# Performance work log

Hardware: AMD Instinct MI355X
Metric: run time of the kernel (lower is better)

## Reference

```python
import jax, jax.numpy as jnp
import numpy as np

B, S, D, H, DK, F, K = 8, 1024, 512, 8, 64, 2048, 31
EPS = 1e-5


def _ln(x, g, b):
    m = jnp.mean(x, -1, keepdims=True)
    v = jnp.mean((x - m) ** 2, -1, keepdims=True)
    return (x - m) * jax.lax.rsqrt(v + EPS) * g + b


def _ff(x, w1, b1, w2, b2):
    return jnp.maximum(x @ w1 + b1, 0.0) @ w2 + b2


def setup_inputs() -> dict:
    key = jax.random.key(0)
    ks = jax.random.split(key, 16)
    w = lambda k, shape: jax.random.normal(k, shape, dtype=jnp.float32) * 0.02
    inp = {"x": jax.random.normal(ks[0], (B, S, D), dtype=jnp.float32)}
    for name in ["norm1", "norm2", "norm3", "norm4", "conv_ln"]:
        inp[name + "_g"] = jnp.ones((D,), jnp.float32)
        inp[name + "_b"] = jnp.zeros((D,), jnp.float32)
    # feed-forward 1 and 2
    inp["ff1_w1"] = w(ks[1], (D, F)); inp["ff1_b1"] = jnp.zeros((F,), jnp.float32)
    inp["ff1_w2"] = w(ks[2], (F, D)); inp["ff1_b2"] = jnp.zeros((D,), jnp.float32)
    inp["ff2_w1"] = w(ks[3], (D, F)); inp["ff2_b1"] = jnp.zeros((F,), jnp.float32)
    inp["ff2_w2"] = w(ks[4], (F, D)); inp["ff2_b2"] = jnp.zeros((D,), jnp.float32)
    # attention projections ([in, out] layout)
    inp["wq"] = w(ks[5], (D, D)); inp["bq"] = jnp.zeros((D,), jnp.float32)
    inp["wk"] = w(ks[6], (D, D)); inp["bk"] = jnp.zeros((D,), jnp.float32)
    inp["wv"] = w(ks[7], (D, D)); inp["bv"] = jnp.zeros((D,), jnp.float32)
    inp["wo"] = w(ks[8], (D, D)); inp["bo"] = jnp.zeros((D,), jnp.float32)
    # convolution module
    inp["pw1_w"] = w(ks[9], (D, 2 * D)); inp["pw1_b"] = jnp.zeros((2 * D,), jnp.float32)
    inp["dw_w"] = w(ks[10], (D, 1, K)); inp["dw_b"] = jnp.zeros((D,), jnp.float32)
    inp["bn_g"] = jnp.ones((D,), jnp.float32); inp["bn_b"] = jnp.zeros((D,), jnp.float32)
    inp["bn_mean"] = jnp.zeros((D,), jnp.float32); inp["bn_var"] = jnp.ones((D,), jnp.float32)
    inp["pw2_w"] = w(ks[11], (D, D)); inp["pw2_b"] = jnp.zeros((D,), jnp.float32)
    return inp


def _forward(x, norm1_g, norm1_b, norm2_g, norm2_b, norm3_g, norm3_b, norm4_g, norm4_b,
             ff1_w1, ff1_b1, ff1_w2, ff1_b2, wq, bq, wk, bk, wv, bv, wo, bo,
             conv_ln_g, conv_ln_b, pw1_w, pw1_b, dw_w, dw_b,
             bn_g, bn_b, bn_mean, bn_var, pw2_w, pw2_b,
             ff2_w1, ff2_b1, ff2_w2, ff2_b2):
    b, s, _ = x.shape
    # half-step FF1
    x = x + 0.5 * _ff(_ln(x, norm1_g, norm1_b), ff1_w1, ff1_b1, ff1_w2, ff1_b2)
    # multi-head self-attention (pre-norm)
    h = _ln(x, norm2_g, norm2_b)
    q = (h @ wq + bq).reshape(b, s, H, DK)
    k = (h @ wk + bk).reshape(b, s, H, DK)
    v = (h @ wv + bv).reshape(b, s, H, DK)
    scores = jnp.einsum("bqhd,bkhd->bhqk", q, k) / jnp.sqrt(jnp.asarray(DK, x.dtype))
    attn = jax.nn.softmax(scores, axis=-1)
    o = jnp.einsum("bhqk,bkhd->bqhd", attn, v).reshape(b, s, D)
    x = x + (o @ wo + bo)
    # convolution module (pre-norm)
    h = _ln(x, norm3_g, norm3_b)
    h = _ln(h, conv_ln_g, conv_ln_b)
    h = h @ pw1_w + pw1_b                                 # [B,S,2D] pointwise conv1
    h = h[..., :D] * jax.nn.sigmoid(h[..., D:])           # GLU over channels
    h = h.transpose(0, 2, 1)                              # [B,D,S]
    h = jax.lax.conv_general_dilated(
        h, dw_w, window_strides=(1,), padding=((K // 2, K // 2),),
        feature_group_count=D, dimension_numbers=("NCH", "OIH", "NCH")) + dw_b[:, None]
    h = (h - bn_mean[:, None]) * jax.lax.rsqrt(bn_var + EPS)[:, None] * bn_g[:, None] + bn_b[:, None]
    h = h * jax.nn.sigmoid(h)                             # SiLU
    h = jnp.einsum("bcl,co->bol", h, pw2_w) + pw2_b[:, None]
    x = x + h.transpose(0, 2, 1)
    # half-step FF2
    x = x + 0.5 * _ff(_ln(x, norm4_g, norm4_b), ff2_w1, ff2_b1, ff2_w2, ff2_b2)
    return x


def reference(x, norm1_g, norm1_b, norm2_g, norm2_b, norm3_g, norm3_b, norm4_g, norm4_b,
              conv_ln_g, conv_ln_b, ff1_w1, ff1_b1, ff1_w2, ff1_b2,
              ff2_w1, ff2_b1, ff2_w2, ff2_b2, wq, bq, wk, bk, wv, bv, wo, bo,
              pw1_w, pw1_b, dw_w, dw_b, bn_g, bn_b, bn_mean, bn_var, pw2_w, pw2_b):
    return _forward(x, norm1_g, norm1_b, norm2_g, norm2_b, norm3_g, norm3_b, norm4_g, norm4_b,
                    ff1_w1, ff1_b1, ff1_w2, ff1_b2, wq, bq, wk, bk, wv, bv, wo, bo,
                    conv_ln_g, conv_ln_b, pw1_w, pw1_b, dw_w, dw_b,
                    bn_g, bn_b, bn_mean, bn_var, pw2_w, pw2_b,
                    ff2_w1, ff2_b1, ff2_w2, ff2_b2)
```

## Files before the change

### kernel.cpp

```cpp
#include <hip/hip_runtime.h>
#include <math.h>

#define TOK    8192
#define DMODEL 512
#define FDIM   2048
#define NH     8
#define DKH    64
#define SEQ    1024
#define BATCH  8
#define KCONV  31
#define LN_EPS 1e-5f

typedef __attribute__((ext_vector_type(8))) short bf16x8;
typedef __attribute__((ext_vector_type(4))) float f32x4;
typedef unsigned short ushort_t;

#define AS1 __attribute__((address_space(1)))
#define AS3 __attribute__((address_space(3)))

#define QSCALE 0.1803368801111204f

__device__ __forceinline__ float sigf(float x) { return 1.0f / (1.0f + __expf(-x)); }

__device__ __forceinline__ unsigned short f2bf(float f) {
  unsigned u = __float_as_uint(f);
  u = u + 0x7fffu + ((u >> 16) & 1u);
  return (unsigned short)(u >> 16);
}
__device__ __forceinline__ unsigned pk2(float a, float b) {
  return (unsigned)f2bf(a) | ((unsigned)f2bf(b) << 16);
}
__device__ __forceinline__ float bf2f(ushort_t u) {
  return __uint_as_float((unsigned)u << 16);
}

__device__ __forceinline__ void xcd_swizzle(int gx, int* bx, int* by) {
  const int nwg = gx * (int)gridDim.y;
  const int cpx = nwg >> 3;
  const int bid = (*by) * gx + (*bx);
  const int wg = (bid & 7) * cpx + (bid >> 3);
  *bx = wg % gx;
  *by = wg / gx;
}

struct WJob { const float* src; ushort_t* dst; int K, N, t0; };
struct WJobs {
  WJob j[10];
  int misc_t0;
  const float* dww; const float* bq; const float* bk; const float* bv;
  float* wTc; float* bcat;
};

__global__ __launch_bounds__(256) void wcast_all(WJobs jobs) {
  __shared__ float tile[32][33];
  const int t = blockIdx.x;
  const int tx = threadIdx.x, ty = threadIdx.y;
  if (t >= jobs.misc_t0) {
    const int idx = (t - jobs.misc_t0) * 256 + ty * 32 + tx;
    if (idx < DMODEL * KCONV) {
      const int d = idx / KCONV, k = idx % KCONV;
      jobs.wTc[k * DMODEL + d] = jobs.dww[idx];
    } else if (idx < DMODEL * KCONV + 3 * DMODEL) {
      const int c = idx - DMODEL * KCONV;
      jobs.bcat[c] = (c < DMODEL) ? jobs.bq[c]
                    : (c < 2 * DMODEL ? jobs.bk[c - DMODEL] : jobs.bv[c - 2 * DMODEL]);
    }
    return;
  }
  int i = 0;
#pragma unroll
  for (int k = 1; k < 10; ++k) if (t >= jobs.j[k].t0) i = k;
  const WJob jb = jobs.j[i];
  const int local = t - jb.t0;
  const int ntx = jb.N >> 5;
  const int bx = (local % ntx) * 32, by = (local / ntx) * 32;
#pragma unroll
  for (int r = 0; r < 32; r += 8)
    tile[ty + r][tx] = jb.src[(size_t)(by + ty + r) * jb.N + bx + tx];
  __syncthreads();
#pragma unroll
  for (int r = 0; r < 32; r += 8)
    jb.dst[(size_t)(bx + ty + r) * jb.K + by + tx] = f2bf(tile[tx][ty + r]);
}

template <bool OBF>
__global__ __launch_bounds__(256) void ln_kernel(const float* __restrict__ in,
                                                 const float* __restrict__ g,
                                                 const float* __restrict__ b,
                                                 void* __restrict__ outp) {
  const int wave = threadIdx.x >> 6, lane = threadIdx.x & 63;
  const size_t row = (size_t)blockIdx.x * 4 + wave;
  const float* p = in + row * DMODEL + lane * 8;
  const float4 v0 = *(const float4*)p;
  const float4 v1 = *(const float4*)(p + 4);
  float s  = v0.x + v0.y + v0.z + v0.w + v1.x + v1.y + v1.z + v1.w;
  float ss = v0.x*v0.x + v0.y*v0.y + v0.z*v0.z + v0.w*v0.w
           + v1.x*v1.x + v1.y*v1.y + v1.z*v1.z + v1.w*v1.w;
#pragma unroll
  for (int m = 1; m < 64; m <<= 1) { s += __shfl_xor(s, m); ss += __shfl_xor(ss, m); }
  const float mean = s * (1.0f / DMODEL);
  const float var  = ss * (1.0f / DMODEL) - mean * mean;
  const float rstd = rsqrtf(var + LN_EPS);
  const float4 g0 = *(const float4*)(g + lane * 8);
  const float4 g1 = *(const float4*)(g + lane * 8 + 4);
  const float4 bb0 = *(const float4*)(b + lane * 8);
  const float4 bb1 = *(const float4*)(b + lane * 8 + 4);
  float o[8];
  o[0] = (v0.x - mean) * rstd * g0.x + bb0.x;
  o[1] = (v0.y - mean) * rstd * g0.y + bb0.y;
  o[2] = (v0.z - mean) * rstd * g0.z + bb0.z;
  o[3] = (v0.w - mean) * rstd * g0.w + bb0.w;
  o[4] = (v1.x - mean) * rstd * g1.x + bb1.x;
  o[5] = (v1.y - mean) * rstd * g1.y + bb1.y;
  o[6] = (v1.z - mean) * rstd * g1.z + bb1.z;
  o[7] = (v1.w - mean) * rstd * g1.w + bb1.w;
  if (OBF) {
    uint4 pkv;
    pkv.x = pk2(o[0], o[1]); pkv.y = pk2(o[2], o[3]);
    pkv.z = pk2(o[4], o[5]); pkv.w = pk2(o[6], o[7]);
    *(uint4*)((ushort_t*)outp + row * DMODEL + lane * 8) = pkv;
  } else {
    float4 a, c;
    a.x = o[0]; a.y = o[1]; a.z = o[2]; a.w = o[3];
    c.x = o[4]; c.y = o[5]; c.z = o[6]; c.w = o[7];
    float* q = (float*)outp + row * DMODEL + lane * 8;
    *(float4*)q = a;
    *(float4*)(q + 4) = c;
  }
}

__global__ __launch_bounds__(256) void ln2_kernel(const float* __restrict__ in,
                                                  const float* __restrict__ g1,
                                                  const float* __restrict__ b1,
                                                  const float* __restrict__ g2,
                                                  const float* __restrict__ b2,
                                                  ushort_t* __restrict__ outp) {
  const int wave = threadIdx.x >> 6, lane = threadIdx.x & 63;
  const size_t row = (size_t)blockIdx.x * 4 + wave;
  const float* p = in + row * DMODEL + lane * 8;
  float v[8];
  {
    const float4 v0 = *(const float4*)p;
    const float4 v1 = *(const float4*)(p + 4);
    v[0]=v0.x; v[1]=v0.y; v[2]=v0.z; v[3]=v0.w;
    v[4]=v1.x; v[5]=v1.y; v[6]=v1.z; v[7]=v1.w;
  }
  float s = 0.f, ss = 0.f;
#pragma unroll
  for (int e = 0; e < 8; ++e) { s += v[e]; ss += v[e]*v[e]; }
#pragma unroll
  for (int m = 1; m < 64; m <<= 1) { s += __shfl_xor(s, m); ss += __shfl_xor(ss, m); }
  float mean = s * (1.0f / DMODEL);
  float rstd = rsqrtf(ss * (1.0f / DMODEL) - mean * mean + LN_EPS);
  const float4 ga = *(const float4*)(g1 + lane * 8);
  const float4 gb = *(const float4*)(g1 + lane * 8 + 4);
  const float4 ba = *(const float4*)(b1 + lane * 8);
  const float4 bb = *(const float4*)(b1 + lane * 8 + 4);
  const float gg1[8] = {ga.x,ga.y,ga.z,ga.w,gb.x,gb.y,gb.z,gb.w};
  const float bb1[8] = {ba.x,ba.y,ba.z,ba.w,bb.x,bb.y,bb.z,bb.w};
#pragma unroll
  for (int e = 0; e < 8; ++e) v[e] = (v[e] - mean) * rstd * gg1[e] + bb1[e];
  s = 0.f; ss = 0.f;
#pragma unroll
  for (int e = 0; e < 8; ++e) { s += v[e]; ss += v[e]*v[e]; }
#pragma unroll
  for (int m = 1; m < 64; m <<= 1) { s += __shfl_xor(s, m); ss += __shfl_xor(ss, m); }
  mean = s * (1.0f / DMODEL);
  rstd = rsqrtf(ss * (1.0f / DMODEL) - mean * mean + LN_EPS);
  const float4 gc = *(const float4*)(g2 + lane * 8);
  const float4 gd = *(const float4*)(g2 + lane * 8 + 4);
  const float4 bc = *(const float4*)(b2 + lane * 8);
  const float4 bd = *(const float4*)(b2 + lane * 8 + 4);
  const float gg2[8] = {gc.x,gc.y,gc.z,gc.w,gd.x,gd.y,gd.z,gd.w};
  const float bb2[8] = {bc.x,bc.y,bc.z,bc.w,bd.x,bd.y,bd.z,bd.w};
  float o[8];
#pragma unroll
  for (int e = 0; e < 8; ++e) o[e] = (v[e] - mean) * rstd * gg2[e] + bb2[e];
  uint4 pkv;
  pkv.x = pk2(o[0], o[1]); pkv.y = pk2(o[2], o[3]);
  pkv.z = pk2(o[4], o[5]); pkv.w = pk2(o[6], o[7]);
  *(uint4*)(outp + row * DMODEL + lane * 8) = pkv;
}

template <int ACT, bool QSC>
__global__ __launch_bounds__(512, 2) void gemm256(const ushort_t* __restrict__ A,
                                                  const ushort_t* __restrict__ Bt,
                                                  const float* __restrict__ bias,
                                                  ushort_t* __restrict__ Cout,
                                                  int N) {
  __shared__ ushort_t lds[65536];
  const int t = threadIdx.x;
  const int l = t & 63;
  const int wid = t >> 6;
  const int wm = wid >> 2, wn = wid & 3;
  int bx = blockIdx.x, by = blockIdx.y;
  xcd_swizzle(gridDim.x, &bx, &by);
  const int m0 = by * 256, n0 = bx * 256;
  const int K = 512;

  f32x4 acc[8][4];
#pragma unroll
  for (int m = 0; m < 8; ++m)
#pragma unroll
    for (int n = 0; n < 4; ++n) acc[m][n] = (f32x4){0.f, 0.f, 0.f, 0.f};

  const int srow = t >> 3;
  const int schunk = (t & 7) ^ ((t >> 3) & 7);

#define STAGE_A(TAU, C_, I_)                                                    \
  __builtin_amdgcn_global_load_lds(                                             \
      (const AS1 unsigned*)(A + (size_t)(m0 + (I_) * 64 + srow) * K +           \
                            (TAU) * 64 + schunk * 8),                           \
      (AS3 unsigned*)(lds + (C_) * 16384 + ((I_) * 512 + t) * 8), 16, 0, 0)
#define STAGE_B(TAU, C_, I_)                                                    \
  __builtin_amdgcn_global_load_lds(                                             \
      (const AS1 unsigned*)(Bt + (size_t)(n0 + (I_) * 64 + srow) * K +          \
                            (TAU) * 64 + schunk * 8),                           \
      (AS3 unsigned*)(lds + 32768 + (C_) * 16384 + ((I_) * 512 + t) * 8), 16, 0, 0)

#pragma unroll
  for (int i = 0; i < 4; ++i) STAGE_B(0, 0, i);
#pragma unroll
  for (int i = 0; i < 4; ++i) STAGE_A(0, 0, i);
#pragma unroll
  for (int i = 0; i < 4; ++i) STAGE_B(1, 1, i);
  STAGE_A(1, 1, 0);
  STAGE_A(1, 1, 2);
  asm volatile("s_waitcnt vmcnt(6)" ::: "memory");
  __builtin_amdgcn_s_barrier();

  const int arow = (l & 15);
  const int kch0 = (l >> 4);
  bf16x8 bfr[2][4];

  for (int it = 0; it < 4; ++it) {
    const bool stg = (it < 3);
#pragma unroll
    for (int h = 0; h < 2; ++h) {
      const int c = h;
#pragma unroll
      for (int p = 0; p < 4; ++p) {
        bf16x8 afr[2][2];
#pragma unroll
        for (int m2 = 0; m2 < 2; ++m2)
#pragma unroll
          for (int ks = 0; ks < 2; ++ks) {
            const int row = wm * 128 + (2 * p + m2) * 16 + arow;
            const int ch = (ks * 4 + kch0) ^ (row & 7);
            afr[m2][ks] = *(const bf16x8*)(lds + c * 16384 + row * 64 + ch * 8);
          }
        if (p == 0) {
#pragma unroll
          for (int nr = 0; nr < 4; ++nr)
#pragma unroll
            for (int ks = 0; ks < 2; ++ks) {
              const int row = wn * 64 + nr * 16 + arow;
              const int ch = (ks * 4 + kch0) ^ (row & 7);
              bfr[ks][nr] = *(const bf16x8*)(lds + 32768 + c * 16384 + row * 64 + ch * 8);
            }
        }
        if (p == 0) {
          if (h == 0 || stg) {
            STAGE_A(2 * it + h + 1, c ^ 1, 1);
            STAGE_A(2 * it + h + 1, c ^ 1, 3);
          }
        } else if (p == 1) {
          if (stg) {
#pragma unroll
            for (int i = 0; i < 4; ++i) STAGE_B(2 * it + h + 2, c, i);
          }
        } else if (p == 2) {
          if (stg) {
            STAGE_A(2 * it + h + 2, c, 0);
            STAGE_A(2 * it + h + 2, c, 2);
          }
        }
        __builtin_amdgcn_s_barrier();
        __builtin_amdgcn_s_setprio(1);
#pragma unroll
        for (int ks = 0; ks < 2; ++ks)
#pragma unroll
          for (int m2 = 0; m2 < 2; ++m2)
#pragma unroll
            for (int nr = 0; nr < 4; ++nr)
              acc[2 * p + m2][nr] = __builtin_amdgcn_mfma_f32_16x16x32_bf16(
                  afr[m2][ks], bfr[ks][nr], acc[2 * p + m2][nr], 0, 0, 0);
        __builtin_amdgcn_s_setprio(0);
        if (p == 3) {
          if (h == 0) {
            if (stg) asm volatile("s_waitcnt vmcnt(6)" ::: "memory");
            else     asm volatile("s_waitcnt vmcnt(0)" ::: "memory");
          } else if (stg) {
            asm volatile("s_waitcnt vmcnt(6)" ::: "memory");
          }
        }
        __builtin_amdgcn_s_barrier();
      }
    }
  }
#undef STAGE_A
#undef STAGE_B

#pragma unroll
  for (int m = 0; m < 8; ++m) {
    const int row_b = m0 + wm * 128 + m * 16 + (l >> 4) * 4;
#pragma unroll
    for (int n = 0; n < 4; ++n) {
      const int col = n0 + wn * 64 + n * 16 + (l & 15);
      const float bv = bias[col];
      const float sc = QSC ? (col < DMODEL ? QSCALE : 1.0f) : 1.0f;
#pragma unroll
      for (int j = 0; j < 4; ++j) {
        float v = acc[m][n][j] + bv;
        if (ACT == 1) v = fmaxf(v, 0.f);
        v *= sc;
        Cout[(size_t)(row_b + j) * N + col] = f2bf(v);
      }
    }
  }
}

template <int TN, int ACT, bool RES, bool OBF, bool QSC>
__global__ __launch_bounds__(256) void gemm_bf16(const ushort_t* __restrict__ A,
                                                 const ushort_t* __restrict__ Bt,
                                                 const float* __restrict__ bias,
                                                 const float* __restrict__ Rp,
                                                 float alpha,
                                                 void* __restrict__ Cout,
                                                 int M, int N, int K) {
  constexpr int NF = TN / 32;
  constexpr int NB = TN / 32;
  __shared__ ushort_t Al[128 * 64];
  __shared__ ushort_t Bl[TN * 64];
  const int t = threadIdx.x;
  const int lane = t & 63;
  const int wid = t >> 6;
  const int wr = wid >> 1, wc = wid & 1;
  int bx = blockIdx.x, by = blockIdx.y;
  xcd_swizzle(gridDim.x, &bx, &by);
  const int m0 = by * 128, n0 = bx * TN;

  f32x4 acc[4][NF];
#pragma unroll
  for (int m = 0; m < 4; ++m)
#pragma unroll
    for (int n = 0; n < NF; ++n) acc[m][n] = (f32x4){0.f, 0.f, 0.f, 0.f};

  const int srow = t >> 3;
  const int scol = (t & 7) * 8;
  const ushort_t* Ag = A + (size_t)(m0 + srow) * K + scol;
  const ushort_t* Bg = Bt + (size_t)(n0 + srow) * K + scol;

  for (int k0 = 0; k0 < K; k0 += 64) {
    __syncthreads();
#pragma unroll
    for (int i = 0; i < 4; ++i) {
      __builtin_amdgcn_global_load_lds(
          (const AS1 unsigned*)(Ag + (size_t)i * 32 * K + k0),
          (AS3 unsigned*)(Al + ((size_t)i * 256 + t) * 8),
          16, 0, 0);
    }
#pragma unroll
    for (int i = 0; i < NB; ++i) {
      __builtin_amdgcn_global_load_lds(
          (const AS1 unsigned*)(Bg + (size_t)i * 32 * K + k0),
          (AS3 unsigned*)(Bl + ((size_t)i * 256 + t) * 8),
          16, 0, 0);
    }
    __syncthreads();

#pragma unroll
    for (int ks = 0; ks < 2; ++ks) {
      const int kk = ks * 32 + (lane >> 4) * 8;
      bf16x8 af[4], bfv[NF];
#pragma unroll
      for (int m = 0; m < 4; ++m)
        af[m] = *(const bf16x8*)(Al + (wr * 64 + m * 16 + (lane & 15)) * 64 + kk);
#pragma unroll
      for (int n = 0; n < NF; ++n)
        bfv[n] = *(const bf16x8*)(Bl + (wc * (TN / 2) + n * 16 + (lane & 15)) * 64 + kk);
#pragma unroll
      for (int m = 0; m < 4; ++m)
#pragma unroll
        for (int n = 0; n < NF; ++n)
          acc[m][n] = __builtin_amdgcn_mfma_f32_16x16x32_bf16(af[m], bfv[n], acc[m][n], 0, 0, 0);
    }
  }

#pragma unroll
  for (int m = 0; m < 4; ++m) {
    const int row_b = m0 + wr * 64 + m * 16 + (lane >> 4) * 4;
#pragma unroll
    for (int n = 0; n < NF; ++n) {
      const int col = n0 + wc * (TN / 2) + n * 16 + (lane & 15);
      const float bv = bias[col];
#pragma unroll
      for (int j = 0; j < 4; ++j) {
        float v = acc[m][n][j] + bv;
        if (ACT == 1) v = fmaxf(v, 0.f);
        if (QSC) v *= (col < DMODEL ? QSCALE : 1.0f);
        const size_t idx = (size_t)(row_b + j) * N + col;
        if (RES) v = Rp[idx] + alpha * v;
        if (OBF) ((ushort_t*)Cout)[idx] = f2bf(v);
        else     ((float*)Cout)[idx] = v;
      }
    }
  }
}

__global__ __launch_bounds__(256) void gemm_glu(const ushort_t* __restrict__ A,
                                                const ushort_t* __restrict__ Bt,
                                                const float* __restrict__ bias,
                                                ushort_t* __restrict__ Cout) {
  __shared__ ushort_t Al[128 * 64];
  __shared__ ushort_t Bl[128 * 64];
  const int t = threadIdx.x;
  const int lane = t & 63;
  const int wid = t >> 6;
  const int wr = wid >> 1, wc = wid & 1;
  int bx = blockIdx.x, by = blockIdx.y;
  xcd_swizzle(gridDim.x, &bx, &by);
  const int m0 = by * 128, n0 = bx * 64;
  const int K = DMODEL, N = DMODEL;

  f32x4 aa[4][2], ag[4][2];
#pragma unroll
  for (int m = 0; m < 4; ++m)
#pragma unroll
    for (int n = 0; n < 2; ++n) {
      aa[m][n] = (f32x4){0.f, 0.f, 0.f, 0.f};
      ag[m][n] = (f32x4){0.f, 0.f, 0.f, 0.f};
    }

  const int srow = t >> 3;
  const int scol = (t & 7) * 8;
  const ushort_t* Ag_ = A + (size_t)(m0 + srow) * K + scol;
  const ushort_t* Ba_ = Bt + (size_t)(n0 + srow) * K + scol;
  const ushort_t* Bg_ = Bt + (size_t)(512 + n0 + srow) * K + scol;

  for (int k0 = 0; k0 < K; k0 += 64) {
    __syncthreads();
#pragma unroll
    for (int i = 0; i < 4; ++i) {
      __builtin_amdgcn_global_load_lds(
          (const AS1 unsigned*)(Ag_ + (size_t)i * 32 * K + k0),
          (AS3 unsigned*)(Al + ((size_t)i * 256 + t) * 8),
          16, 0, 0);
    }
#pragma unroll
    for (int i = 0; i < 2; ++i) {
      __builtin_amdgcn_global_load_lds(
          (const AS1 unsigned*)(Ba_ + (size_t)i * 32 * K + k0),
          (AS3 unsigned*)(Bl + ((size_t)i * 256 + t) * 8),
          16, 0, 0);
      __builtin_amdgcn_global_load_lds(
          (const AS1 unsigned*)(Bg_ + (size_t)i * 32 * K + k0),
          (AS3 unsigned*)(Bl + 64 * 64 + ((size_t)i * 256 + t) * 8),
          16, 0, 0);
    }
    __syncthreads();

#pragma unroll
    for (int ks = 0; ks < 2; ++ks) {
      const int kk = ks * 32 + (lane >> 4) * 8;
      bf16x8 af[4], bfa[2], bfg[2];
#pragma unroll
      for (int m = 0; m < 4; ++m)
        af[m] = *(const bf16x8*)(Al + (wr * 64 + m * 16 + (lane & 15)) * 64 + kk);
#pragma unroll
      for (int n = 0; n < 2; ++n) {
        bfa[n] = *(const bf16x8*)(Bl + (wc * 32 + n * 16 + (lane & 15)) * 64 + kk);
        bfg[n] = *(const bf16x8*)(Bl + (64 + wc * 32 + n * 16 + (lane & 15)) * 64 + kk);
      }
#pragma unroll
      for (int m = 0; m < 4; ++m)
#pragma unroll
        for (int n = 0; n < 2; ++n) {
          aa[m][n] = __builtin_amdgcn_mfma_f32_16x16x32_bf16(af[m], bfa[n], aa[m][n], 0, 0, 0);
          ag[m][n] = __builtin_amdgcn_mfma_f32_16x16x32_bf16(af[m], bfg[n], ag[m][n], 0, 0, 0);
        }
    }
  }

#pragma unroll
  for (int m = 0; m < 4; ++m) {
    const int row_b = m0 + wr * 64 + m * 16 + (lane >> 4) * 4;
#pragma unroll
    for (int n = 0; n < 2; ++n) {
      const int col = n0 + wc * 32 + n * 16 + (lane & 15);
      const float ba_v = bias[col];
      const float bg_v = bias[col + DMODEL];
#pragma unroll
      for (int j = 0; j < 4; ++j) {
        const float av = aa[m][n][j] + ba_v;
        const float gv = ag[m][n][j] + bg_v;
        Cout[(size_t)(row_b + j) * N + col] = f2bf(av * sigf(gv));
      }
    }
  }
}

__global__ __launch_bounds__(256) void vtrans(const ushort_t* __restrict__ QKV,
                                              ushort_t* __restrict__ Vt) {
  __shared__ ushort_t tl[64][72];
  const int st = blockIdx.x;
  const int bh = blockIdx.y;
  const int b = bh >> 3, h = bh & 7;
  const int t = threadIdx.x;
#pragma unroll
  for (int i = 0; i < 2; ++i) {
    const int chunk = i * 256 + t;
    const int sr = chunk >> 3, c8 = (chunk & 7) * 8;
    *(uint4*)&tl[sr][c8] =
        *(const uint4*)(QKV + ((size_t)(b * SEQ + st * 64 + sr) * (3 * DMODEL)) + 2 * DMODEL + h * DKH + c8);
  }
  __syncthreads();
#pragma unroll
  for (int i = 0; i < 2; ++i) {
    const int chunk = i * 256 + t;
    const int dr = chunk >> 3, c8 = (chunk & 7) * 8;
    ushort_t tmp[8];
#pragma unroll
    for (int e = 0; e < 8; ++e) tmp[e] = tl[c8 + e][dr];
    *(uint4*)(Vt + ((size_t)(bh * DKH + dr) * SEQ) + st * 64 + c8) = *(uint4*)tmp;
  }
}

__global__ __launch_bounds__(256) void attn_mfma(const ushort_t* __restrict__ QKV,
                                                 const ushort_t* __restrict__ Vt,
                                                 ushort_t* __restrict__ Om) {
  __shared__ ushort_t Ks[128 * 64];
  __shared__ ushort_t Vs[64 * 128];
  __shared__ ushort_t Ps[64 * 128];
  const int t = threadIdx.x;
  const int l = t & 63;
  const int w = t >> 6;
  const int qb = blockIdx.x, h = blockIdx.y, b = blockIdx.z;
  const size_t rowstr = 3 * DMODEL;
  const size_t baseQ = ((size_t)b * SEQ) * rowstr + (size_t)h * DKH;
  const size_t baseK = baseQ + DMODEL;
  const size_t baseV = (size_t)(b * NH + h) * DKH * SEQ;
  const size_t baseO = ((size_t)b * SEQ) * DMODEL + (size_t)h * DKH;

  bf16x8 qf[2];
  {
    const int qrow = qb * 64 + w * 16 + (l & 15);
    const ushort_t* qp = QKV + baseQ + (size_t)qrow * rowstr + ((l >> 4) * 8);
    qf[0] = *(const bf16x8*)(qp);
    qf[1] = *(const bf16x8*)(qp + 32);
  }

  const int krr = t >> 3, kch = t & 7;
  const int vrr = t >> 4, vch = t & 15;

  float mrun[4], lrun[4];
  f32x4 o[4];
#pragma unroll
  for (int j = 0; j < 4; ++j) { mrun[j] = -1e30f; lrun[j] = 0.f; }
#pragma unroll
  for (int n = 0; n < 4; ++n) o[n] = (f32x4){0.f, 0.f, 0.f, 0.f};

  for (int kt = 0; kt < SEQ / 128; ++kt) {
    __syncthreads();
#pragma unroll
    for (int i = 0; i < 4; ++i) {
      const int r = i * 32 + krr;
      __builtin_amdgcn_global_load_lds(
          (const AS1 unsigned*)
              (QKV + baseK + (size_t)(kt * 128 + r) * rowstr + ((kch ^ (r & 7)) * 8)),
          (AS3 unsigned*)(Ks + ((size_t)i * 256 + t) * 8),
          16, 0, 0);
    }
#pragma unroll
    for (int i = 0; i < 4; ++i) {
      const int r = i * 16 + vrr;
      __builtin_amdgcn_global_load_lds(
          (const AS1 unsigned*)
              (Vt + baseV + (size_t)r * SEQ + kt * 128 + ((vch ^ (r & 15)) * 8)),
          (AS3 unsigned*)(Vs + ((size_t)i * 256 + t) * 8),
          16, 0, 0);
    }
    __syncthreads();

    f32x4 s[8];
#pragma unroll
    for (int n = 0; n < 8; ++n) s[n] = (f32x4){0.f, 0.f, 0.f, 0.f};
    __builtin_amdgcn_s_setprio(1);
#pragma unroll
    for (int ks = 0; ks < 2; ++ks) {
      const int kk = ks * 64 + (l >> 4) * 16;
#pragma unroll
      for (int n = 0; n < 8; ++n) {
        const int krow = n * 16 + (l & 15);
        const bf16x8 kf = *(const bf16x8*)((char*)Ks + krow * 128 + (kk ^ ((krow & 7) << 4)));
        s[n] = __builtin_amdgcn_mfma_f32_16x16x32_bf16(qf[ks], kf, s[n], 0, 0, 0);
      }
    }
    __builtin_amdgcn_s_setprio(0);

#pragma unroll
    for (int j = 0; j < 4; ++j) {
      float r0 = fmaxf(fmaxf(fmaxf(s[0][j], s[1][j]), fmaxf(s[2][j], s[3][j])),
                       fmaxf(fmaxf(s[4][j], s[5][j]), fmaxf(s[6][j], s[7][j])));
      r0 = fmaxf(r0, __shfl_xor(r0, 1));
      r0 = fmaxf(r0, __shfl_xor(r0, 2));
      r0 = fmaxf(r0, __shfl_xor(r0, 4));
      r0 = fmaxf(r0, __shfl_xor(r0, 8));
      const float mn = fmaxf(mrun[j], r0);
      const float cs = exp2f(mrun[j] - mn);
      const int prow = w * 16 + (l >> 4) * 4 + j;
      const int pswz = (prow & 15) << 4;
      float psum = 0.f;
#pragma unroll
      for (int n = 0; n < 8; ++n) {
        const float p = exp2f(s[n][j] - mn);
        psum += p;
        const int col2 = (n * 16 + (l & 15)) * 2;
        *(ushort_t*)((char*)Ps + prow * 256 + (col2 ^ pswz)) = f2bf(p);
      }
      psum += __shfl_xor(psum, 1);
      psum += __shfl_xor(psum, 2);
      psum += __shfl_xor(psum, 4);
      psum += __shfl_xor(psum, 8);
      lrun[j] = lrun[j] * cs + psum;
      mrun[j] = mn;
      o[0][j] *= cs; o[1][j] *= cs; o[2][j] *= cs; o[3][j] *= cs;
    }

    __builtin_amdgcn_s_setprio(1);
#pragma unroll
    for (int ks = 0; ks < 4; ++ks) {
      const int kk = ks * 64 + (l >> 4) * 16;
      const int arow = w * 16 + (l & 15);
      const bf16x8 pf = *(const bf16x8*)((char*)Ps + arow * 256 + (kk ^ ((arow & 15) << 4)));
#pragma unroll
      for (int n = 0; n < 4; ++n) {
        const int vrow = n * 16 + (l & 15);
        const bf16x8 vf = *(const bf16x8*)((char*)Vs + vrow * 256 + (kk ^ ((vrow & 15) << 4)));
        o[n] = __builtin_amdgcn_mfma_f32_16x16x32_bf16(pf, vf, o[n], 0, 0, 0);
      }
    }
    __builtin_amdgcn_s_setprio(0);
  }

  float inv[4];
#pragma unroll
  for (int j = 0; j < 4; ++j) inv[j] = 1.0f / lrun[j];
#pragma unroll
  for (int j = 0; j < 4; ++j) {
    const int prow = w * 16 + (l >> 4) * 4 + j;
    const int pswz = (prow & 15) << 4;
#pragma unroll
    for (int n = 0; n < 4; ++n) {
      const int col2 = (n * 16 + (l & 15)) * 2;
      *(ushort_t*)((char*)Ps + prow * 256 + (col2 ^ pswz)) = f2bf(o[n][j] * inv[j]);
    }
  }
  __syncthreads();
#pragma unroll
  for (int i = 0; i < 2; ++i) {
    const int chunk = i * 256 + t;
    const int qr = chunk >> 3, c8 = (chunk & 7) * 8;
    const uint4 ov = *(const uint4*)((char*)Ps + qr * 256 + ((c8 * 2) ^ ((qr & 15) << 4)));
    *(uint4*)(Om + baseO + (size_t)(qb * 64 + qr) * DMODEL + c8) = ov;
  }
}

__global__ __launch_bounds__(256) void dwconv_bn_silu(const ushort_t* __restrict__ in,
                                                      const float* __restrict__ wT,
                                                      const float* __restrict__ dwb,
                                                      const float* __restrict__ bng,
                                                      const float* __restrict__ bnb,
                                                      const float* __restrict__ bnm,
                                                      const float* __restrict__ bnv,
                                                      ushort_t* __restrict__ out) {
  const size_t gid = (size_t)blockIdx.x * 256 + threadIdx.x;
  const int dc = (int)(gid & 63) * 8;
  const int s = (int)((gid >> 6) & (SEQ - 1));
  const int b = (int)(gid >> 16);
  const ushort_t* bp = in + (size_t)b * SEQ * DMODEL;
  float a[8];
#pragma unroll
  for (int e = 0; e < 8; ++e) a[e] = 0.f;
#pragma unroll
  for (int k = 0; k < KCONV; ++k) {
    const int ssi = s + k - (KCONV / 2);
    if (ssi < 0 || ssi >= SEQ) continue;
    ushort_t xv[8];
    *(uint4*)xv = *(const uint4*)(bp + (size_t)ssi * DMODEL + dc);
    const float4 w0 = *(const float4*)(wT + k * DMODEL + dc);
    const float4 w1 = *(const float4*)(wT + k * DMODEL + dc + 4);
    a[0] = fmaf(bf2f(xv[0]), w0.x, a[0]); a[1] = fmaf(bf2f(xv[1]), w0.y, a[1]);
    a[2] = fmaf(bf2f(xv[2]), w0.z, a[2]); a[3] = fmaf(bf2f(xv[3]), w0.w, a[3]);
    a[4] = fmaf(bf2f(xv[4]), w1.x, a[4]); a[5] = fmaf(bf2f(xv[5]), w1.y, a[5]);
    a[6] = fmaf(bf2f(xv[6]), w1.z, a[6]); a[7] = fmaf(bf2f(xv[7]), w1.w, a[7]);
  }
  float v[8];
#pragma unroll
  for (int half = 0; half < 2; ++half) {
    const int d4 = dc + half * 4;
    const float4 bi = *(const float4*)(dwb + d4);
    const float4 mm = *(const float4*)(bnm + d4);
    const float4 vv = *(const float4*)(bnv + d4);
    const float4 gg = *(const float4*)(bng + d4);
    const float4 b2 = *(const float4*)(bnb + d4);
    const float bia[4] = {bi.x, bi.y, bi.z, bi.w};
    const float mma[4] = {mm.x, mm.y, mm.z, mm.w};
    const float vva[4] = {vv.x, vv.y, vv.z, vv.w};
    const float gga[4] = {gg.x, gg.y, gg.z, gg.w};
    const float b2a[4] = {b2.x, b2.y, b2.z, b2.w};
#pragma unroll
    for (int e = 0; e < 4; ++e) {
      float t0 = a[half * 4 + e] + bia[e];
      t0 = (t0 - mma[e]) * rsqrtf(vva[e] + LN_EPS) * gga[e] + b2a[e];
      v[half * 4 + e] = t0 * sigf(t0);
    }
  }
  uint4 o;
  o.x = pk2(v[0], v[1]); o.y = pk2(v[2], v[3]);
  o.z = pk2(v[4], v[5]); o.w = pk2(v[6], v[7]);
  *(uint4*)&out[(((size_t)b * SEQ + s) * DMODEL) + dc] = o;
}

extern "C" void kernel_launch(void* const* d_in, const int* in_sizes, int n_in,
                              void* d_out, int out_size, void* d_ws, size_t ws_size,
                              hipStream_t stream) {
  const float* x    = (const float*)d_in[0];
  const float* n1g  = (const float*)d_in[1];
  const float* n1b  = (const float*)d_in[2];
  const float* n2g  = (const float*)d_in[3];
  const float* n2b  = (const float*)d_in[4];
  const float* n3g  = (const float*)d_in[5];
  const float* n3b  = (const float*)d_in[6];
  const float* n4g  = (const float*)d_in[7];
  const float* n4b  = (const float*)d_in[8];
  const float* clg  = (const float*)d_in[9];
  const float* clb  = (const float*)d_in[10];
  const float* f1w1 = (const float*)d_in[11];
  const float* f1b1 = (const float*)d_in[12];
  const float* f1w2 = (const float*)d_in[13];
  const float* f1b2 = (const float*)d_in[14];
  const float* f2w1 = (const float*)d_in[15];
  const float* f2b1 = (const float*)d_in[16];
  const float* f2w2 = (const float*)d_in[17];
  const float* f2b2 = (const float*)d_in[18];
  const float* wq   = (const float*)d_in[19];
  const float* bq   = (const float*)d_in[20];
  const float* wk   = (const float*)d_in[21];
  const float* bk   = (const float*)d_in[22];
  const float* wv   = (const float*)d_in[23];
  const float* bv   = (const float*)d_in[24];
  const float* wo   = (const float*)d_in[25];
  const float* bo   = (const float*)d_in[26];
  const float* pw1w = (const float*)d_in[27];
  const float* pw1b = (const float*)d_in[28];
  const float* dww  = (const float*)d_in[29];
  const float* dwb  = (const float*)d_in[30];
  const float* bng  = (const float*)d_in[31];
  const float* bnb  = (const float*)d_in[32];
  const float* bnm  = (const float*)d_in[33];
  const float* bnv  = (const float*)d_in[34];
  const float* pw2w = (const float*)d_in[35];
  const float* pw2b = (const float*)d_in[36];

  char* wsb = (char*)d_ws;
  const size_t MB = 1ull << 20;
  ushort_t* Wbf    = (ushort_t*)(wsb + 0);
  ushort_t* f1w1T  = Wbf + 0;
  ushort_t* f1w2T  = Wbf + (1ull << 20);
  ushort_t* f2w1T  = Wbf + (2ull << 20);
  ushort_t* f2w2T  = Wbf + (3ull << 20);
  ushort_t* wqkvT  = Wbf + (4ull << 20);
  ushort_t* wkT    = wqkvT + (256ull << 10);
  ushort_t* wvT    = wqkvT + (512ull << 10);
  ushort_t* woT    = wqkvT + (768ull << 10);
  ushort_t* pw1T   = Wbf + (5ull << 20);
  ushort_t* pw2T   = Wbf + (5ull << 20) + (512ull << 10);
  float*    WTc    = (float*)(wsb + 12 * MB);
  float*    bcat   = (float*)(wsb + 12 * MB + 128 * 1024);
  ushort_t* Lbf    = (ushort_t*)(wsb + 13 * MB);
  ushort_t* Hbf    = (ushort_t*)(wsb + 21 * MB);
  ushort_t* QKVb   = (ushort_t*)(wsb + 53 * MB);
  ushort_t* Vtb    = (ushort_t*)(wsb + 77 * MB);
  ushort_t* Gbf    = (ushort_t*)(wsb + 53 * MB);
  ushort_t* Obf    = (ushort_t*)(wsb + 85 * MB);
  ushort_t* Cbf    = Obf;
  float* out = (float*)d_out;

  const dim3 blk(256);
  const dim3 blk512(512);
  const dim3 blkT(32, 8);
  const dim3 gLN(TOK / 4);
  const dim3 gFFa256(FDIM / 256, TOK / 256);
  const dim3 gQKV256(3 * DMODEL / 256, TOK / 256);
  const dim3 gFFb(DMODEL / 64, TOK / 128);
  const dim3 gGLU(DMODEL / 64, TOK / 128);
  const dim3 gAttn(SEQ / 64, NH, BATCH);
  const dim3 gVt(SEQ / 64, BATCH * NH);
  const dim3 gConv(TOK * 64 / 256);

  {
    WJobs jobs;
    const float* srcs[10] = {f1w1, f1w2, f2w1, f2w2, wq, wk, wv, wo, pw1w, pw2w};
    ushort_t* dsts[10] = {f1w1T, f1w2T, f2w1T, f2w2T, wqkvT, wkT, wvT, woT, pw1T, pw2T};
    const int Ks[10] = {512, 2048, 512, 2048, 512, 512, 512, 512, 512, 512};
    const int Ns[10] = {2048, 512, 2048, 512, 512, 512, 512, 512, 1024, 512};
    int t0 = 0;
    for (int i = 0; i < 10; ++i) {
      jobs.j[i].src = srcs[i]; jobs.j[i].dst = dsts[i];
      jobs.j[i].K = Ks[i]; jobs.j[i].N = Ns[i]; jobs.j[i].t0 = t0;
      t0 += (Ks[i] / 32) * (Ns[i] / 32);
    }
    jobs.misc_t0 = t0;
    jobs.dww = dww; jobs.bq = bq; jobs.bk = bk; jobs.bv = bv;
    jobs.wTc = WTc; jobs.bcat = bcat;
    const int nmisc = (DMODEL * KCONV + 3 * DMODEL + 255) / 256;
    wcast_all<<<t0 + nmisc, blkT, 0, stream>>>(jobs);
  }

  ln_kernel<true><<<gLN, blk, 0, stream>>>(x, n1g, n1b, Lbf);
  gemm256<1, false><<<gFFa256, blk512, 0, stream>>>(Lbf, f1w1T, f1b1, Hbf, FDIM);
  gemm_bf16<64,  0, true,  false, false><<<gFFb, blk, 0, stream>>>(Hbf, f1w2T, f1b2, x, 0.5f, out, TOK, DMODEL, FDIM);

  ln_kernel<true><<<gLN, blk, 0, stream>>>(out, n2g, n2b, Lbf);
  gemm256<0, true><<<gQKV256, blk512, 0, stream>>>(Lbf, wqkvT, bcat, QKVb, 3 * DMODEL);
  vtrans<<<gVt, blk, 0, stream>>>(QKVb, Vtb);
  attn_mfma<<<gAttn, blk, 0, stream>>>(QKVb, Vtb, Obf);
  gemm_bf16<64,  0, true,  false, false><<<gFFb, blk, 0, stream>>>(Obf, woT, bo, out, 1.0f, out, TOK, DMODEL, DMODEL);

  ln2_kernel<<<gLN, blk, 0, stream>>>(out, n3g, n3b, clg, clb, Lbf);
  gemm_glu<<<gGLU, blk, 0, stream>>>(Lbf, pw1T, pw1b, Gbf);
  dwconv_bn_silu<<<gConv, blk, 0, stream>>>(Gbf, WTc, dwb, bng, bnb, bnm, bnv, Cbf);
  gemm_bf16<64,  0, true,  false, false><<<gFFb, blk, 0, stream>>>(Cbf, pw2T, pw2b, out, 1.0f, out, TOK, DMODEL, DMODEL);

  ln_kernel<true><<<gLN, blk, 0, stream>>>(out, n4g, n4b, Lbf);
  gemm256<1, false><<<gFFa256, blk512, 0, stream>>>(Lbf, f2w1T, f2b1, Hbf, FDIM);
  gemm_bf16<64,  0, true,  false, false><<<gFFb, blk, 0, stream>>>(Hbf, f2w2T, f2b2, out, 0.5f, out, TOK, DMODEL, FDIM);
}
```

Baseline: 311.0 us.

## Double-buffer K/V tiles in attention and use native exp2 intrinsic

The attention kernel now keeps two LDS buffers for K and V. It issues the async global-to-LDS loads for the next key tile before computing on the current one, and needs only one barrier per iteration. The aim is to hide global load latency behind the QK and PV MFMA work. Softmax exponentials also switch from exp2f to the hardware exp2 builtin, which drops the range-handling code. In exchange, LDS use per block rises to about 64KB, which can lower occupancy.

After: 307.6 us. About the same (-1.1%).

```diff
diff --git a/kernel.cpp b/kernel.cpp
--- a/kernel.cpp
+++ b/kernel.cpp
@@ -21,6 +21,7 @@
 #define QSCALE 0.1803368801111204f
 
 __device__ __forceinline__ float sigf(float x) { return 1.0f / (1.0f + __expf(-x)); }
+__device__ __forceinline__ float exp2n(float x) { return __builtin_amdgcn_exp2f(x); }
 
 __device__ __forceinline__ unsigned short f2bf(float f) {
   unsigned u = __float_as_uint(f);
@@ -529,8 +530,8 @@
 __global__ __launch_bounds__(256) void attn_mfma(const ushort_t* __restrict__ QKV,
                                                  const ushort_t* __restrict__ Vt,
                                                  ushort_t* __restrict__ Om) {
-  __shared__ ushort_t Ks[128 * 64];
-  __shared__ ushort_t Vs[64 * 128];
+  __shared__ ushort_t Ks[2][128 * 64];
+  __shared__ ushort_t Vs[2][64 * 128];
   __shared__ ushort_t Ps[64 * 128];
   const int t = threadIdx.x;
   const int l = t & 63;
@@ -553,6 +554,26 @@
   const int krr = t >> 3, kch = t & 7;
   const int vrr = t >> 4, vch = t & 15;
 
+#define STAGE_KV(KT, BUF)                                                       \
+  {                                                                             \
+    _Pragma("unroll")                                                           \
+    for (int i = 0; i < 4; ++i) {                                               \
+      const int r = i * 32 + krr;                                               \
+      __builtin_amdgcn_global_load_lds(                                         \
+          (const AS1 unsigned*)(QKV + baseK +                                   \
+              (size_t)((KT) * 128 + r) * rowstr + ((kch ^ (r & 7)) * 8)),       \
+          (AS3 unsigned*)(Ks[BUF] + ((size_t)i * 256 + t) * 8), 16, 0, 0);      \
+    }                                                                           \
+    _Pragma("unroll")                                                           \
+    for (int i = 0; i < 4; ++i) {                                               \
+      const int r = i * 16 + vrr;                                               \
+      __builtin_amdgcn_global_load_lds(                                         \
+          (const AS1 unsigned*)(Vt + baseV +                                    \
+              (size_t)r * SEQ + (KT) * 128 + ((vch ^ (r & 15)) * 8)),           \
+          (AS3 unsigned*)(Vs[BUF] + ((size_t)i * 256 + t) * 8), 16, 0, 0);      \
+    }                                                                           \
+  }
+
   float mrun[4], lrun[4];
   f32x4 o[4];
 #pragma unroll
@@ -560,27 +581,15 @@
 #pragma unroll
   for (int n = 0; n < 4; ++n) o[n] = (f32x4){0.f, 0.f, 0.f, 0.f};
 
+  STAGE_KV(0, 0);
+  __syncthreads();
+
+  int cur = 0;
   for (int kt = 0; kt < SEQ / 128; ++kt) {
-    __syncthreads();
-#pragma unroll
-    for (int i = 0; i < 4; ++i) {
-      const int r = i * 32 + krr;
-      __builtin_amdgcn_global_load_lds(
-          (const AS1 unsigned*)
-              (QKV + baseK + (size_t)(kt * 128 + r) * rowstr + ((kch ^ (r & 7)) * 8)),
-          (AS3 unsigned*)(Ks + ((size_t)i * 256 + t) * 8),
-          16, 0, 0);
-    }
-#pragma unroll
-    for (int i = 0; i < 4; ++i) {
-      const int r = i * 16 + vrr;
-      __builtin_amdgcn_global_load_lds(
-          (const AS1 unsigned*)
-              (Vt + baseV + (size_t)r * SEQ + kt * 128 + ((vch ^ (r & 15)) * 8)),
-          (AS3 unsigned*)(Vs + ((size_t)i * 256 + t) * 8),
-          16, 0, 0);
-    }
-    __syncthreads();
+    if (kt + 1 < SEQ / 128) STAGE_KV(kt + 1, cur ^ 1);
+
+    const ushort_t* Kc = Ks[cur];
+    const ushort_t* Vc = Vs[cur];
 
     f32x4 s[8];
 #pragma unroll
@@ -592,7 +601,7 @@
 #pragma unroll
       for (int n = 0; n < 8; ++n) {
         const int krow = n * 16 + (l & 15);
-        const bf16x8 kf = *(const bf16x8*)((char*)Ks + krow * 128 + (kk ^ ((krow & 7) << 4)));
+        const bf16x8 kf = *(const bf16x8*)((const char*)Kc + krow * 128 + (kk ^ ((krow & 7) << 4)));
         s[n] = __builtin_amdgcn_mfma_f32_16x16x32_bf16(qf[ks], kf, s[n], 0, 0, 0);
       }
     }
@@ -607,13 +616,13 @@
       r0 = fmaxf(r0, __shfl_xor(r0, 4));
       r0 = fmaxf(r0, __shfl_xor(r0, 8));
       const float mn = fmaxf(mrun[j], r0);
-      const float cs = exp2f(mrun[j] - mn);
+      const float cs = exp2n(mrun[j] - mn);
       const int prow = w * 16 + (l >> 4) * 4 + j;
       const int pswz = (prow & 15) << 4;
       float psum = 0.f;
 #pragma unroll
       for (int n = 0; n < 8; ++n) {
-        const float p = exp2f(s[n][j] - mn);
+        const float p = exp2n(s[n][j] - mn);
         psum += p;
         const int col2 = (n * 16 + (l & 15)) * 2;
         *(ushort_t*)((char*)Ps + prow * 256 + (col2 ^ pswz)) = f2bf(p);
@@ -636,12 +645,16 @@
 #pragma unroll
       for (int n = 0; n < 4; ++n) {
         const int vrow = n * 16 + (l & 15);
-        const bf16x8 vf = *(const bf16x8*)((char*)Vs + vrow * 256 + (kk ^ ((vrow & 15) << 4)));
+        const bf16x8 vf = *(const bf16x8*)((const char*)Vc + vrow * 256 + (kk ^ ((vrow & 15) << 4)));
         o[n] = __builtin_amdgcn_mfma_f32_16x16x32_bf16(pf, vf, o[n], 0, 0, 0);
       }
     }
     __builtin_amdgcn_s_setprio(0);
-  }
+
+    __syncthreads();
+    cur ^= 1;
+  }
+#undef STAGE_KV
 
   float inv[4];
 #pragma unroll
```
